# Optimization experiments

Hardware: AMD Instinct MI355X
Metric: run time of the kernel (lower is better)

Reference implementation:

```python
import jax, jax.numpy as jnp
import numpy as np

VOCAB, EMB, HID, T, B, NCLS = 50000, 300, 512, 128, 256, 3


def _lstm_final_h(x, lens, W, b):
    """TF BasicLSTMCell semantics (gate order i,j,f,o; forget_bias=1.0) with
    dynamic_rnn sequence_length masking; returns final hidden state [B, HID].
    x: [B, T, EMB] float, lens: [B] int, W: [EMB+HID, 4*HID], b: [4*HID].
    """
    xt = jnp.swapaxes(x, 0, 1)                       # [T, B, EMB]
    mask = jnp.arange(T)[:, None] < lens[None, :]    # [T, B]

    def step(carry, inp):
        c, h = carry
        x_t, m = inp
        z = jnp.concatenate([x_t, h], axis=-1) @ W + b   # [B, 4*HID]
        i, j, f, o = jnp.split(z, 4, axis=-1)
        c_new = c * jax.nn.sigmoid(f + 1.0) + jax.nn.sigmoid(i) * jnp.tanh(j)
        h_new = jnp.tanh(c_new) * jax.nn.sigmoid(o)
        m = m[:, None]
        return (jnp.where(m, c_new, c), jnp.where(m, h_new, h)), None

    init = (jnp.zeros((x.shape[0], HID), x.dtype),
            jnp.zeros((x.shape[0], HID), x.dtype))
    (c, h), _ = jax.lax.scan(step, init, (xt, mask))
    return h


def setup_inputs() -> dict:
    key = jax.random.key(0)
    ks = jax.random.split(key, 12)
    s = 0.05
    return {
        "left_ids": jax.random.randint(ks[0], (B, T), 0, VOCAB, dtype=jnp.int32),
        "right_ids": jax.random.randint(ks[1], (B, T), 0, VOCAB, dtype=jnp.int32),
        "left_len": jax.random.randint(ks[2], (B,), 1, T + 1, dtype=jnp.int32),
        "right_len": jax.random.randint(ks[3], (B,), 1, T + 1, dtype=jnp.int32),
        "embeddings": jax.random.normal(ks[4], (VOCAB, EMB), jnp.float32) * s,
        "W_l": jax.random.normal(ks[5], (EMB + HID, 4 * HID), jnp.float32) * s,
        "b_l": jnp.zeros((4 * HID,), jnp.float32),
        "W_r": jax.random.normal(ks[6], (EMB + HID, 4 * HID), jnp.float32) * s,
        "b_r": jnp.zeros((4 * HID,), jnp.float32),
        "W_d": jax.random.normal(ks[7], (2 * HID, NCLS), jnp.float32) * s,
        "b_d": jnp.zeros((NCLS,), jnp.float32),
    }


def reference(left_ids, right_ids, left_len, right_len,
              embeddings, W_l, b_l, W_r, b_r, W_d, b_d):
    left_x = embeddings[left_ids]      # [B, T, EMB]
    right_x = embeddings[right_ids]    # [B, T, EMB]
    h_l = _lstm_final_h(left_x, left_len, W_l, b_l)     # [B, HID]
    h_r = _lstm_final_h(right_x, right_len, W_r, b_r)   # [B, HID]
    logits = jnp.concatenate([h_l, h_r], axis=1) @ W_d + b_d  # [B, NCLS]
    return logits
```

## Files before the change

### kernel.cpp

```cpp
#include <hip/hip_runtime.h>


using bf16x8 = __attribute__((ext_vector_type(8))) __bf16;
using f32x4  = __attribute__((ext_vector_type(4))) float;
using u32x4  = __attribute__((ext_vector_type(4))) unsigned int;
typedef unsigned short u16;
typedef unsigned long long u64;

#define NT 128
#define ROWB 1664
#define SWZ(row, off) ((off) ^ (((row) & 7) << 4))

#define LGKM0  asm volatile("s_waitcnt lgkmcnt(0)" ::: "memory")
#define VM0    asm volatile("s_waitcnt vmcnt(0)" ::: "memory")
#define BAR()  __builtin_amdgcn_s_barrier()
#define SCHED0 __builtin_amdgcn_sched_barrier(0)

__device__ __forceinline__ u16 f2bf(float f) {
  union { float f; unsigned u; } v; v.f = f;
  unsigned r = v.u + 0x7fffu + ((v.u >> 16) & 1u);
  return (u16)(r >> 16);
}
__device__ __forceinline__ float sigf(float x) { return 1.f / (1.f + __expf(-x)); }
__device__ __forceinline__ float tanhf_(float x) { return 2.f / (1.f + __expf(-2.f * x)) - 1.f; }

__device__ __forceinline__ void setA26(bf16x8 (&A)[26], int kt, bf16x8 v) {
  switch (kt) {
    case 0:A[0]=v;break;  case 1:A[1]=v;break;  case 2:A[2]=v;break;
    case 3:A[3]=v;break;  case 4:A[4]=v;break;  case 5:A[5]=v;break;
    case 6:A[6]=v;break;  case 7:A[7]=v;break;  case 8:A[8]=v;break;
    case 9:A[9]=v;break;  case 10:A[10]=v;break; case 11:A[11]=v;break;
    case 12:A[12]=v;break; case 13:A[13]=v;break; case 14:A[14]=v;break;
    case 15:A[15]=v;break; case 16:A[16]=v;break; case 17:A[17]=v;break;
    case 18:A[18]=v;break; case 19:A[19]=v;break; case 20:A[20]=v;break;
    case 21:A[21]=v;break; case 22:A[22]=v;break; case 23:A[23]=v;break;
    case 24:A[24]=v;break; case 25:A[25]=v;break;
  }
}

__global__ __launch_bounds__(256, 1) void lstm_persist(
    const int* __restrict__ lids, const int* __restrict__ rids,
    const int* __restrict__ llen, const int* __restrict__ rlen,
    const float* __restrict__ emb,
    const float* __restrict__ Wl, const float* __restrict__ bl,
    const float* __restrict__ Wr, const float* __restrict__ br,
    u64* __restrict__ hbuf,
    float* __restrict__ hfin,
    unsigned int* __restrict__ bar)
{
  __shared__ __align__(16) unsigned char sB[32 * ROWB];
  __shared__ __align__(8)  u16 sH[32][36];
  __shared__ int sI[4096];

  const int tid = threadIdx.x;
  const int w = tid >> 6, l = tid & 63;
  const int bid = blockIdx.x;
  const int xcd = bid & 7, idx = bid >> 3;
  const int grp = xcd * 2 + (idx >> 4);
  const int ct  = idx & 15;
  const int lstm = grp >> 3, bt = grp & 7;
  const int b0 = bt * 32, u0 = ct * 32;

  const int*   ids  = lstm ? rids : lids;
  const int*   lenp = lstm ? rlen : llen;
  const float* W    = lstm ? Wr : Wl;
  const float* bv   = lstm ? br : bl;
  unsigned int* const blp = bar + grp * 32;

  bf16x8 A0[26], A1[26];
  {
    float* sW = (float*)sB;
    for (int kc = 0; kc < 13; ++kc) {
      for (int i = 0; i < 32; ++i) {
        int id2 = tid + i * 256;
        int c = id2 & 31, r = (id2 >> 5) & 63, g = id2 >> 11;
        int kk = kc * 64 + r;
        float v = 0.f;
        if (kk < 300)       v = W[kk * 2048 + g * 512 + u0 + c];
        else if (kk >= 320) v = W[(kk - 20) * 2048 + g * 512 + u0 + c];
        sW[(g * 64 + r) * 32 + c] = v;
      }
      __syncthreads();
      #pragma unroll
      for (int kt2 = 0; kt2 < 2; ++kt2) {
        int kt = kc * 2 + kt2;
        #pragma unroll
        for (int mf2 = 0; mf2 < 2; ++mf2) {
          int mf = w * 2 + mf2;
          int rho = mf * 16 + (l & 15);
          int du = rho >> 2, g = rho & 3;
          union { u16 s[8]; bf16x8 v; } tmp;
          #pragma unroll
          for (int j = 0; j < 8; ++j) {
            int kr = kt2 * 32 + ((l >> 4) << 3) + j;
            tmp.s[j] = f2bf(sW[(g * 64 + kr) * 32 + du]);
          }
          if (mf2 == 0) setA26(A0, kt, tmp.v); else setA26(A1, kt, tmp.v);
        }
      }
      __syncthreads();
    }
  }

  if (tid < 160) {
    int row = tid / 5, c5 = tid - (tid / 5) * 5;
    *(u64*)(sB + row * ROWB + SWZ(row, 600 + c5 * 8)) = 0ULL;
  }
  {
    const int* src = ids + b0 * NT;
    #pragma unroll
    for (int i = 0; i < 4; ++i)
      *(int4*)&sI[(tid + i * 256) * 4] = *(const int4*)&src[(tid + i * 256) * 4];
  }

  int ldsoff[10], sirow[10], foff[10];
  #pragma unroll
  for (int i = 0; i < 10; ++i) {
    int id2 = tid + i * 256;
    int row = id2 / 75, f4 = id2 - row * 75;
    ldsoff[i] = row * ROWB + SWZ(row, f4 * 8);
    sirow[i]  = row * NT;
    foff[i]   = f4 * 4;
  }
  int hoff[16];
  #pragma unroll
  for (int i = 0; i < 16; ++i) {
    int id2 = tid + i * 256;
    int row = id2 >> 7, c8 = id2 & 127;
    hoff[i] = row * ROWB + SWZ(row, 640 + c8 * 8);
  }

  int lenn[2];
  lenn[0] = lenp[b0 + (l & 15)];
  lenn[1] = lenp[b0 + 16 + (l & 15)];
  float bia[2][4];
  #pragma unroll
  for (int mf2 = 0; mf2 < 2; ++mf2) {
    int du = w * 8 + mf2 * 4 + (l >> 4);
    #pragma unroll
    for (int g = 0; g < 4; ++g) bia[mf2][g] = bv[g * 512 + u0 + du];
  }
  float cst[2][2] = {{0.f, 0.f}, {0.f, 0.f}};
  float hst[2][2] = {{0.f, 0.f}, {0.f, 0.f}};
  __syncthreads();

  float4 px[10];
  #pragma unroll
  for (int i = 0; i < 10; ++i)
    if (i < 9 || tid < 96) {
      int eid = sI[sirow[i]];
      float4 xv = *(const float4*)(emb + eid * 300 + foff[i]);
      u64 pk = (u64)f2bf(xv.x) | ((u64)f2bf(xv.y) << 16) |
               ((u64)f2bf(xv.z) << 32) | ((u64)f2bf(xv.w) << 48);
      *(u64*)(sB + ldsoff[i]) = pk;
    }
  #pragma unroll
  for (int i = 0; i < 10; ++i)
    if (i < 9 || tid < 96) {
      int eid = sI[sirow[i] + 1];
      px[i] = *(const float4*)(emb + eid * 300 + foff[i]);
    }
  __syncthreads();

  const int r0 = l & 15, r1 = 16 + (l & 15);

  f32x4 xacc[2][2];
  xacc[0][0] = {0.f,0.f,0.f,0.f}; xacc[0][1] = {0.f,0.f,0.f,0.f};
  xacc[1][0] = {0.f,0.f,0.f,0.f}; xacc[1][1] = {0.f,0.f,0.f,0.f};
  #pragma unroll
  for (int kt = 0; kt < 10; ++kt) {
    int kb = kt * 64 + ((l >> 4) << 4);
    bf16x8 B0 = __builtin_bit_cast(bf16x8, *(const u32x4*)(sB + r0 * ROWB + SWZ(r0, kb)));
    bf16x8 B1 = __builtin_bit_cast(bf16x8, *(const u32x4*)(sB + r1 * ROWB + SWZ(r1, kb)));
    xacc[0][0] = __builtin_amdgcn_mfma_f32_16x16x32_bf16(A0[kt], B0, xacc[0][0], 0, 0, 0);
    xacc[0][1] = __builtin_amdgcn_mfma_f32_16x16x32_bf16(A0[kt], B1, xacc[0][1], 0, 0, 0);
    xacc[1][0] = __builtin_amdgcn_mfma_f32_16x16x32_bf16(A1[kt], B0, xacc[1][0], 0, 0, 0);
    xacc[1][1] = __builtin_amdgcn_mfma_f32_16x16x32_bf16(A1[kt], B1, xacc[1][1], 0, 0, 0);
  }

  for (int t = 0; t < NT; ++t) {
    if (t > 0) {
      if (tid == 0) {
        unsigned target = 16u * (unsigned)t;
        while (__hip_atomic_load(blp, __ATOMIC_RELAXED, __HIP_MEMORY_SCOPE_AGENT) < target)
          __builtin_amdgcn_s_sleep(1);
      }
      BAR(); SCHED0;
      const u64* hsrc = hbuf + (((lstm * 2 + ((t & 1) ^ 1)) * 256) + b0) * 128;
      u64 hld[16];
      #pragma unroll
      for (int i = 0; i < 16; ++i)
        hld[i] = __hip_atomic_load(&hsrc[tid + i * 256], __ATOMIC_RELAXED,
                                   __HIP_MEMORY_SCOPE_AGENT);
      #pragma unroll
      for (int i = 0; i < 16; ++i) *(u64*)(sB + hoff[i]) = hld[i];
      LGKM0; BAR(); SCHED0;
      #pragma unroll
      for (int kt = 10; kt < 26; ++kt) {
        int kb = kt * 64 + ((l >> 4) << 4);
        bf16x8 B0 = __builtin_bit_cast(bf16x8, *(const u32x4*)(sB + r0 * ROWB + SWZ(r0, kb)));
        bf16x8 B1 = __builtin_bit_cast(bf16x8, *(const u32x4*)(sB + r1 * ROWB + SWZ(r1, kb)));
        xacc[0][0] = __builtin_amdgcn_mfma_f32_16x16x32_bf16(A0[kt], B0, xacc[0][0], 0, 0, 0);
        xacc[0][1] = __builtin_amdgcn_mfma_f32_16x16x32_bf16(A0[kt], B1, xacc[0][1], 0, 0, 0);
        xacc[1][0] = __builtin_amdgcn_mfma_f32_16x16x32_bf16(A1[kt], B0, xacc[1][0], 0, 0, 0);
        xacc[1][1] = __builtin_amdgcn_mfma_f32_16x16x32_bf16(A1[kt], B1, xacc[1][1], 0, 0, 0);
      }
    }

    #pragma unroll
    for (int mf2 = 0; mf2 < 2; ++mf2)
      #pragma unroll
      for (int n = 0; n < 2; ++n) {
        f32x4 z = xacc[mf2][n];
        float zi = z[0] + bia[mf2][0];
        float zj = z[1] + bia[mf2][1];
        float zf = z[2] + bia[mf2][2];
        float zo = z[3] + bia[mf2][3];
        float cn = cst[mf2][n] * sigf(zf + 1.f) + sigf(zi) * tanhf_(zj);
        float hn = tanhf_(cn) * sigf(zo);
        if (t < lenn[n]) { cst[mf2][n] = cn; hst[mf2][n] = hn; }
        sH[n * 16 + (l & 15)][w * 8 + mf2 * 4 + (l >> 4)] = f2bf(hst[mf2][n]);
      }
    LGKM0; BAR(); SCHED0;

    {
      int bbL = tid >> 3, u8 = tid & 7;
      u64 pk = *(const u64*)&sH[bbL][u8 * 4];
      u64* hdst = hbuf + (((lstm * 2 + (t & 1)) * 256) + b0 + bbL) * 128 + (u0 >> 2) + u8;
      __hip_atomic_store(hdst, pk, __ATOMIC_RELAXED, __HIP_MEMORY_SCOPE_AGENT);
    }
    #pragma unroll
    for (int i = 0; i < 10; ++i)
      if (i < 9 || tid < 96) {
        float4 xv = px[i];
        u64 pk = (u64)f2bf(xv.x) | ((u64)f2bf(xv.y) << 16) |
                 ((u64)f2bf(xv.z) << 32) | ((u64)f2bf(xv.w) << 48);
        *(u64*)(sB + ldsoff[i]) = pk;
      }
    VM0; LGKM0; BAR();

    if (tid == 0)
      __hip_atomic_fetch_add(blp, 1u, __ATOMIC_RELAXED, __HIP_MEMORY_SCOPE_AGENT);
    SCHED0;

    {
      int tn2 = (t + 2) & (NT - 1);
      #pragma unroll
      for (int i = 0; i < 10; ++i)
        if (i < 9 || tid < 96) {
          int eid = sI[sirow[i] + tn2];
          px[i] = *(const float4*)(emb + eid * 300 + foff[i]);
        }
    }
    xacc[0][0] = {0.f,0.f,0.f,0.f}; xacc[0][1] = {0.f,0.f,0.f,0.f};
    xacc[1][0] = {0.f,0.f,0.f,0.f}; xacc[1][1] = {0.f,0.f,0.f,0.f};
    #pragma unroll
    for (int kt = 0; kt < 10; ++kt) {
      int kb = kt * 64 + ((l >> 4) << 4);
      bf16x8 B0 = __builtin_bit_cast(bf16x8, *(const u32x4*)(sB + r0 * ROWB + SWZ(r0, kb)));
      bf16x8 B1 = __builtin_bit_cast(bf16x8, *(const u32x4*)(sB + r1 * ROWB + SWZ(r1, kb)));
      xacc[0][0] = __builtin_amdgcn_mfma_f32_16x16x32_bf16(A0[kt], B0, xacc[0][0], 0, 0, 0);
      xacc[0][1] = __builtin_amdgcn_mfma_f32_16x16x32_bf16(A0[kt], B1, xacc[0][1], 0, 0, 0);
      xacc[1][0] = __builtin_amdgcn_mfma_f32_16x16x32_bf16(A1[kt], B0, xacc[1][0], 0, 0, 0);
      xacc[1][1] = __builtin_amdgcn_mfma_f32_16x16x32_bf16(A1[kt], B1, xacc[1][1], 0, 0, 0);
    }
  }

  #pragma unroll
  for (int mf2 = 0; mf2 < 2; ++mf2)
    #pragma unroll
    for (int n = 0; n < 2; ++n) {
      int bb = b0 + n * 16 + (l & 15);
      int uu = u0 + w * 8 + mf2 * 4 + (l >> 4);
      hfin[lstm * (256 * 512) + bb * 512 + uu] = hst[mf2][n];
    }
}

__global__ void dense_out(const float* __restrict__ hfin,
                          const float* __restrict__ Wd, const float* __restrict__ bd,
                          float* __restrict__ out) {
  const int b = blockIdx.x, l = threadIdx.x;
  float a0 = 0.f, a1 = 0.f, a2 = 0.f;
  for (int i = l; i < 1024; i += 64) {
    float hv = (i < 512) ? hfin[b * 512 + i] : hfin[256 * 512 + b * 512 + (i - 512)];
    a0 += hv * Wd[i * 3 + 0];
    a1 += hv * Wd[i * 3 + 1];
    a2 += hv * Wd[i * 3 + 2];
  }
  #pragma unroll
  for (int off = 32; off > 0; off >>= 1) {
    a0 += __shfl_down(a0, off);
    a1 += __shfl_down(a1, off);
    a2 += __shfl_down(a2, off);
  }
  if (l == 0) {
    out[b * 3 + 0] = a0 + bd[0];
    out[b * 3 + 1] = a1 + bd[1];
    out[b * 3 + 2] = a2 + bd[2];
  }
}

extern "C" void kernel_launch(void* const* d_in, const int* in_sizes, int n_in,
                              void* d_out, int out_size, void* d_ws, size_t ws_size,
                              hipStream_t stream) {
  const int*   lids = (const int*)d_in[0];
  const int*   rids = (const int*)d_in[1];
  const int*   llen = (const int*)d_in[2];
  const int*   rlen = (const int*)d_in[3];
  const float* emb  = (const float*)d_in[4];
  const float* Wl   = (const float*)d_in[5];
  const float* bl   = (const float*)d_in[6];
  const float* Wr   = (const float*)d_in[7];
  const float* br   = (const float*)d_in[8];
  const float* Wd   = (const float*)d_in[9];
  const float* bd   = (const float*)d_in[10];

  unsigned char* ws = (unsigned char*)d_ws;
  unsigned int* bar = (unsigned int*)ws;
  u64*   hbuf = (u64*)(ws + 4096);
  float* hfin = (float*)(ws + 4096 + (1u << 20));

  hipMemsetAsync(bar, 0, 2048, stream);
  hipLaunchKernelGGL(lstm_persist, dim3(256), dim3(256), 0, stream,
                     lids, rids, llen, rlen, emb, Wl, bl, Wr, br, hbuf, hfin, bar);
  hipLaunchKernelGGL(dense_out, dim3(256), dim3(64), 0, stream,
                     hfin, Wd, bd, (float*)d_out);
}
```

Before: 667.9 us.

## Replace counter barrier with per-element step tags in hidden-state exchange

Drops the global atomic counter barrier between workgroups of the same group. Each bf16 hidden value is now stored with a 16-bit timestep tag, and readers spin until every tag they loaded matches the expected step, which removes the vmcnt drain, the fetch_add and the separate poll. It doubles the size of the hidden exchange buffer and adds a memset of that buffer. The final dense projection is also folded into the persistent kernel as per-tile partial sums, so the follow-up kernel only sums 32 partials per output.

```diff
diff --git a/kernel.cpp b/kernel.cpp
--- a/kernel.cpp
+++ b/kernel.cpp
@@ -5,6 +5,7 @@
 using f32x4  = __attribute__((ext_vector_type(4))) float;
 using u32x4  = __attribute__((ext_vector_type(4))) unsigned int;
 typedef unsigned short u16;
+typedef unsigned int u32;
 typedef unsigned long long u64;
 
 #define NT 128
@@ -12,7 +13,6 @@
 #define SWZ(row, off) ((off) ^ (((row) & 7) << 4))
 
 #define LGKM0  asm volatile("s_waitcnt lgkmcnt(0)" ::: "memory")
-#define VM0    asm volatile("s_waitcnt vmcnt(0)" ::: "memory")
 #define BAR()  __builtin_amdgcn_s_barrier()
 #define SCHED0 __builtin_amdgcn_sched_barrier(0)
 
@@ -44,13 +44,14 @@
     const float* __restrict__ emb,
     const float* __restrict__ Wl, const float* __restrict__ bl,
     const float* __restrict__ Wr, const float* __restrict__ br,
+    const float* __restrict__ Wd,
     u64* __restrict__ hbuf,
-    float* __restrict__ hfin,
-    unsigned int* __restrict__ bar)
+    float* __restrict__ part)
 {
   __shared__ __align__(16) unsigned char sB[32 * ROWB];
   __shared__ __align__(8)  u16 sH[32][36];
   __shared__ int sI[4096];
+  __shared__ float sOut[32][3];
 
   const int tid = threadIdx.x;
   const int w = tid >> 6, l = tid & 63;
@@ -65,7 +66,6 @@
   const int*   lenp = lstm ? rlen : llen;
   const float* W    = lstm ? Wr : Wl;
   const float* bv   = lstm ? br : bl;
-  unsigned int* const blp = bar + grp * 32;
 
   bf16x8 A0[26], A1[26];
   {
@@ -117,17 +117,11 @@
   #pragma unroll
   for (int i = 0; i < 10; ++i) {
     int id2 = tid + i * 256;
-    int row = id2 / 75, f4 = id2 - row * 75;
+    int row = (id2 < 2400) ? id2 / 75 : 0;
+    int f4 = id2 - row * 75;
     ldsoff[i] = row * ROWB + SWZ(row, f4 * 8);
     sirow[i]  = row * NT;
     foff[i]   = f4 * 4;
-  }
-  int hoff[16];
-  #pragma unroll
-  for (int i = 0; i < 16; ++i) {
-    int id2 = tid + i * 256;
-    int row = id2 >> 7, c8 = id2 & 127;
-    hoff[i] = row * ROWB + SWZ(row, 640 + c8 * 8);
   }
 
   int lenn[2];
@@ -180,20 +174,40 @@
 
   for (int t = 0; t < NT; ++t) {
     if (t > 0) {
-      if (tid == 0) {
-        unsigned target = 16u * (unsigned)t;
-        while (__hip_atomic_load(blp, __ATOMIC_RELAXED, __HIP_MEMORY_SCOPE_AGENT) < target)
-          __builtin_amdgcn_s_sleep(1);
-      }
-      BAR(); SCHED0;
-      const u64* hsrc = hbuf + (((lstm * 2 + ((t & 1) ^ 1)) * 256) + b0) * 128;
-      u64 hld[16];
-      #pragma unroll
-      for (int i = 0; i < 16; ++i)
-        hld[i] = __hip_atomic_load(&hsrc[tid + i * 256], __ATOMIC_RELAXED,
-                                   __HIP_MEMORY_SCOPE_AGENT);
-      #pragma unroll
-      for (int i = 0; i < 16; ++i) *(u64*)(sB + hoff[i]) = hld[i];
+      const u32 tagx = (u32)(t - 1);
+      const u64* hsrc = hbuf + (((u64)(lstm * 2 + ((t & 1) ^ 1)) * 256 + b0) * 256);
+      #pragma unroll
+      for (int bi = 0; bi < 2; ++bi) {
+        u64 hv[8][2];
+        bool stale;
+        do {
+          #pragma unroll
+          for (int i = 0; i < 8; ++i) {
+            int lp = tid + (bi * 8 + i) * 256;
+            int row = lp >> 7, c4 = lp & 127;
+            const u64* p = hsrc + row * 256 + c4 * 2;
+            hv[i][0] = __hip_atomic_load(&p[0], __ATOMIC_RELAXED, __HIP_MEMORY_SCOPE_AGENT);
+            hv[i][1] = __hip_atomic_load(&p[1], __ATOMIC_RELAXED, __HIP_MEMORY_SCOPE_AGENT);
+          }
+          u32 acc = 0;
+          #pragma unroll
+          for (int i = 0; i < 8; ++i) {
+            acc |= ((u32)hv[i][0] ^ tagx) & 0xFFFFu;
+            acc |= ((u32)(hv[i][0] >> 32) ^ tagx) & 0xFFFFu;
+            acc |= ((u32)hv[i][1] ^ tagx) & 0xFFFFu;
+            acc |= ((u32)(hv[i][1] >> 32) ^ tagx) & 0xFFFFu;
+          }
+          stale = (acc != 0);
+        } while (__any(stale));
+        #pragma unroll
+        for (int i = 0; i < 8; ++i) {
+          int lp = tid + (bi * 8 + i) * 256;
+          int row = lp >> 7, c4 = lp & 127;
+          u32 lo = ((u32)(hv[i][0] >> 16) & 0xFFFFu) | ((u32)(hv[i][0] >> 32) & 0xFFFF0000u);
+          u32 hi = ((u32)(hv[i][1] >> 16) & 0xFFFFu) | ((u32)(hv[i][1] >> 32) & 0xFFFF0000u);
+          *(u64*)(sB + row * ROWB + SWZ(row, 640 + c4 * 8)) = (u64)lo | ((u64)hi << 32);
+        }
+      }
       LGKM0; BAR(); SCHED0;
       #pragma unroll
       for (int kt = 10; kt < 26; ++kt) {
@@ -224,10 +238,18 @@
     LGKM0; BAR(); SCHED0;
 
     {
-      int bbL = tid >> 3, u8 = tid & 7;
-      u64 pk = *(const u64*)&sH[bbL][u8 * 4];
-      u64* hdst = hbuf + (((lstm * 2 + (t & 1)) * 256) + b0 + bbL) * 128 + (u0 >> 2) + u8;
-      __hip_atomic_store(hdst, pk, __ATOMIC_RELAXED, __HIP_MEMORY_SCOPE_AGENT);
+      int row = tid >> 3, q = tid & 7;
+      u32 tg = (u32)t;
+      u32 v0 = ((u32)sH[row][q * 4 + 0] << 16) | tg;
+      u32 v1 = ((u32)sH[row][q * 4 + 1] << 16) | tg;
+      u32 v2 = ((u32)sH[row][q * 4 + 2] << 16) | tg;
+      u32 v3 = ((u32)sH[row][q * 4 + 3] << 16) | tg;
+      u64* hdst = hbuf + (((u64)(lstm * 2 + (t & 1)) * 256 + b0 + row) * 256)
+                       + (u0 >> 1) + q * 2;
+      __hip_atomic_store(&hdst[0], (u64)v0 | ((u64)v1 << 32),
+                         __ATOMIC_RELAXED, __HIP_MEMORY_SCOPE_AGENT);
+      __hip_atomic_store(&hdst[1], (u64)v2 | ((u64)v3 << 32),
+                         __ATOMIC_RELAXED, __HIP_MEMORY_SCOPE_AGENT);
     }
     #pragma unroll
     for (int i = 0; i < 10; ++i)
@@ -237,11 +259,7 @@
                  ((u64)f2bf(xv.z) << 32) | ((u64)f2bf(xv.w) << 48);
         *(u64*)(sB + ldsoff[i]) = pk;
       }
-    VM0; LGKM0; BAR();
-
-    if (tid == 0)
-      __hip_atomic_fetch_add(blp, 1u, __ATOMIC_RELAXED, __HIP_MEMORY_SCOPE_AGENT);
-    SCHED0;
+    LGKM0; BAR(); SCHED0;
 
     {
       int tn2 = (t + 2) & (NT - 1);
@@ -266,37 +284,34 @@
     }
   }
 
+  if (tid < 96) ((float*)sOut)[tid] = 0.f;
+  __syncthreads();
   #pragma unroll
   for (int mf2 = 0; mf2 < 2; ++mf2)
     #pragma unroll
     for (int n = 0; n < 2; ++n) {
-      int bb = b0 + n * 16 + (l & 15);
+      int row = n * 16 + (l & 15);
       int uu = u0 + w * 8 + mf2 * 4 + (l >> 4);
-      hfin[lstm * (256 * 512) + bb * 512 + uu] = hst[mf2][n];
-    }
-}
-
-__global__ void dense_out(const float* __restrict__ hfin,
-                          const float* __restrict__ Wd, const float* __restrict__ bd,
-                          float* __restrict__ out) {
+      float h = hst[mf2][n];
+      #pragma unroll
+      for (int c = 0; c < 3; ++c)
+        atomicAdd(&sOut[row][c], h * Wd[(lstm * 512 + uu) * 3 + c]);
+    }
+  __syncthreads();
+  if (tid < 96) {
+    int row = tid / 3, c = tid - (tid / 3) * 3;
+    part[(lstm * 16 + ct) * 768 + (b0 + row) * 3 + c] = sOut[row][c];
+  }
+}
+
+__global__ void dense_out(const float* __restrict__ part,
+                          const float* __restrict__ bd, float* __restrict__ out) {
   const int b = blockIdx.x, l = threadIdx.x;
-  float a0 = 0.f, a1 = 0.f, a2 = 0.f;
-  for (int i = l; i < 1024; i += 64) {
-    float hv = (i < 512) ? hfin[b * 512 + i] : hfin[256 * 512 + b * 512 + (i - 512)];
-    a0 += hv * Wd[i * 3 + 0];
-    a1 += hv * Wd[i * 3 + 1];
-    a2 += hv * Wd[i * 3 + 2];
-  }
-  #pragma unroll
-  for (int off = 32; off > 0; off >>= 1) {
-    a0 += __shfl_down(a0, off);
-    a1 += __shfl_down(a1, off);
-    a2 += __shfl_down(a2, off);
-  }
-  if (l == 0) {
-    out[b * 3 + 0] = a0 + bd[0];
-    out[b * 3 + 1] = a1 + bd[1];
-    out[b * 3 + 2] = a2 + bd[2];
+  if (l < 3) {
+    float s = bd[l];
+    #pragma unroll 4
+    for (int k = 0; k < 32; ++k) s += part[k * 768 + b * 3 + l];
+    out[b * 3 + l] = s;
   }
 }
 
@@ -316,13 +331,12 @@
   const float* bd   = (const float*)d_in[10];
 
   unsigned char* ws = (unsigned char*)d_ws;
-  unsigned int* bar = (unsigned int*)ws;
   u64*   hbuf = (u64*)(ws + 4096);
-  float* hfin = (float*)(ws + 4096 + (1u << 20));
-
-  hipMemsetAsync(bar, 0, 2048, stream);
+  float* part = (float*)(ws + 4096 + (2u << 20));
+
+  hipMemsetAsync(hbuf, 0xFF, 2u << 20, stream);
   hipLaunchKernelGGL(lstm_persist, dim3(256), dim3(256), 0, stream,
-                     lids, rids, llen, rlen, emb, Wl, bl, Wr, br, hbuf, hfin, bar);
+                     lids, rids, llen, rlen, emb, Wl, bl, Wr, br, Wd, hbuf, part);
   hipLaunchKernelGGL(dense_out, dim3(256), dim3(64), 0, stream,
-                     hfin, Wd, bd, (float*)d_out);
-}
+                     part, bd, (float*)d_out);
+}
```

Measured after the change: 732.4 us. 9.7% more time.

## Replace atomic counter grid barrier with per-block step flags polled by all waves

Applied to the files above, without the earlier changes.

The shared fetch-add counter per group, polled by one thread and followed by a workgroup barrier, is replaced with per-block flags. Each block stores its step number into its own slot, double-buffered by step parity. Every wave polls all 16 flags of its group with a wave-wide vote, which drops a block barrier from the wait path and removes contention on one atomic counter. It also guards the row computation for out-of-range thread indices. Memory ordering now relies on relaxed flag stores after the barrier and vmcnt wait.

```diff
diff --git a/kernel.cpp b/kernel.cpp
--- a/kernel.cpp
+++ b/kernel.cpp
@@ -5,6 +5,7 @@
 using f32x4  = __attribute__((ext_vector_type(4))) float;
 using u32x4  = __attribute__((ext_vector_type(4))) unsigned int;
 typedef unsigned short u16;
+typedef unsigned int u32;
 typedef unsigned long long u64;
 
 #define NT 128
@@ -46,7 +47,7 @@
     const float* __restrict__ Wr, const float* __restrict__ br,
     u64* __restrict__ hbuf,
     float* __restrict__ hfin,
-    unsigned int* __restrict__ bar)
+    u32* __restrict__ flags)
 {
   __shared__ __align__(16) unsigned char sB[32 * ROWB];
   __shared__ __align__(8)  u16 sH[32][36];
@@ -65,7 +66,6 @@
   const int*   lenp = lstm ? rlen : llen;
   const float* W    = lstm ? Wr : Wl;
   const float* bv   = lstm ? br : bl;
-  unsigned int* const blp = bar + grp * 32;
 
   bf16x8 A0[26], A1[26];
   {
@@ -117,7 +117,8 @@
   #pragma unroll
   for (int i = 0; i < 10; ++i) {
     int id2 = tid + i * 256;
-    int row = id2 / 75, f4 = id2 - row * 75;
+    int row = (id2 < 2400) ? id2 / 75 : 0;
+    int f4 = id2 - row * 75;
     ldsoff[i] = row * ROWB + SWZ(row, f4 * 8);
     sirow[i]  = row * NT;
     foff[i]   = f4 * 4;
@@ -180,12 +181,17 @@
 
   for (int t = 0; t < NT; ++t) {
     if (t > 0) {
-      if (tid == 0) {
-        unsigned target = 16u * (unsigned)t;
-        while (__hip_atomic_load(blp, __ATOMIC_RELAXED, __HIP_MEMORY_SCOPE_AGENT) < target)
-          __builtin_amdgcn_s_sleep(1);
-      }
-      BAR(); SCHED0;
+      {
+        const u32* fl = flags + (grp * 2 + ((t & 1) ^ 1)) * 16;
+        u32 fv; bool ok;
+        do {
+          fv = __hip_atomic_load(&fl[l & 15], __ATOMIC_RELAXED,
+                                 __HIP_MEMORY_SCOPE_AGENT);
+          ok = __all(fv >= (u32)t);
+          if (!ok) __builtin_amdgcn_s_sleep(1);
+        } while (!ok);
+      }
+      SCHED0;
       const u64* hsrc = hbuf + (((lstm * 2 + ((t & 1) ^ 1)) * 256) + b0) * 128;
       u64 hld[16];
       #pragma unroll
@@ -240,7 +246,8 @@
     VM0; LGKM0; BAR();
 
     if (tid == 0)
-      __hip_atomic_fetch_add(blp, 1u, __ATOMIC_RELAXED, __HIP_MEMORY_SCOPE_AGENT);
+      __hip_atomic_store(&flags[(grp * 2 + (t & 1)) * 16 + ct], (u32)(t + 1),
+                         __ATOMIC_RELAXED, __HIP_MEMORY_SCOPE_AGENT);
     SCHED0;
 
     {
@@ -316,13 +323,13 @@
   const float* bd   = (const float*)d_in[10];
 
   unsigned char* ws = (unsigned char*)d_ws;
-  unsigned int* bar = (unsigned int*)ws;
-  u64*   hbuf = (u64*)(ws + 4096);
-  float* hfin = (float*)(ws + 4096 + (1u << 20));
-
-  hipMemsetAsync(bar, 0, 2048, stream);
+  u32*   flags = (u32*)ws;
+  u64*   hbuf  = (u64*)(ws + 4096);
+  float* hfin  = (float*)(ws + 4096 + (1u << 20));
+
+  hipMemsetAsync(flags, 0, 2048, stream);
   hipLaunchKernelGGL(lstm_persist, dim3(256), dim3(256), 0, stream,
-                     lids, rids, llen, rlen, emb, Wl, bl, Wr, br, hbuf, hfin, bar);
+                     lids, rids, llen, rlen, emb, Wl, bl, Wr, br, hbuf, hfin, flags);
   hipLaunchKernelGGL(dense_out, dim3(256), dim3(64), 0, stream,
                      hfin, Wd, bd, (float*)d_out);
 }
```

New measurement: 659.6 us. Within noise of the previous version (-1.2%).
